# Performance work log

Measured on AMD Instinct MI355X. Metric: run time of the kernel, lower is better.

Reference implementation:

```python
import jax, jax.numpy as jnp
import numpy as np

# LIF constants (LIFParams defaults, normalized units)
V_REST = 0.0
V_TH = 1.0
R = 1.0
DT = 1.0
TAU = 10.0
SLOPE = 5.0  # surrogate heaviside slope

N_INPUT, N_HIDDEN, N_OUTPUT = 784, 256, 10
BATCH, T = 128, 500


def setup_inputs() -> dict:
    key = jax.random.key(0)
    k1, k2, k3 = jax.random.split(key, 3)
    input_spikes = jax.random.uniform(k1, (BATCH, N_INPUT, T), dtype=jnp.float32)
    w_input_hidden = jax.random.uniform(k2, (N_INPUT, N_HIDDEN), dtype=jnp.float32) * 0.1
    w_hidden_output = jax.random.uniform(k3, (N_HIDDEN, N_OUTPUT), dtype=jnp.float32) * 0.1
    return {"input_spikes": input_spikes,
            "w_input_hidden": w_input_hidden,
            "w_hidden_output": w_hidden_output}


def reference(input_spikes, w_input_hidden, w_hidden_output):
    # input_spikes: (B, n_input, T)
    batch = input_spikes.shape[0]
    # relu(weight) computed once (original recomputes per step)
    w_ih = jax.nn.relu(w_input_hidden)
    w_ho = jax.nn.relu(w_hidden_output)
    alpha_h = DT / TAU
    alpha_o = DT / TAU

    xs = jnp.transpose(input_spikes, (2, 0, 1))  # (T, B, n_input)

    def step(carry, x_t):
        v_h, v_o = carry
        I_h = x_t @ w_ih                              # (B, n_hidden)
        v_h = v_h + (-(v_h - V_REST) + R * I_h) * alpha_h
        s_h = jax.nn.sigmoid(SLOPE * (v_h - V_TH))
        I_o = s_h @ w_ho                              # (B, n_output)
        v_o = v_o + (-(v_o - V_REST) + R * I_o) * alpha_o
        s_o = jax.nn.sigmoid(SLOPE * (v_o - V_TH))
        return (v_h, v_o), s_o

    v_h0 = jnp.full((batch, N_HIDDEN), V_REST, dtype=input_spikes.dtype)
    v_o0 = jnp.full((batch, N_OUTPUT), V_REST, dtype=input_spikes.dtype)
    _, out_seq = jax.lax.scan(step, (v_h0, v_o0), xs)   # (T, B, n_output)
    output_spikes = jnp.transpose(out_seq, (1, 2, 0))    # (B, n_output, T)
    firing_rates = output_spikes.mean(axis=2)            # (B, n_output)
    return output_spikes, firing_rates
```

## Files before the change

### kernel.cpp

```cpp
#include <hip/hip_runtime.h>


typedef __attribute__((ext_vector_type(4))) float  floatx4;
typedef __attribute__((ext_vector_type(8))) short  shortx8;
typedef unsigned short u16;
typedef unsigned int   u32;

#define B_   128
#define NIN  784
#define NH   256
#define NO   10
#define T_   500
#define NK   25
#define SROW 520

__device__ __forceinline__ u16 f2bf(float f) {
    union { float f; u32 u; } x; x.f = f;
    u32 r = x.u + 0x7FFFu + ((x.u >> 16) & 1u);
    return (u16)(r >> 16);
}
__device__ __forceinline__ float bf2f(u16 u) {
    union { u32 u; float f; } x; x.u = ((u32)u) << 16; return x.f;
}
__device__ __forceinline__ float sigmoid5(float v) {
    return 1.0f / (1.0f + __expf(-5.0f * (v - 1.0f)));
}

__device__ __forceinline__ void gload16(const u16* g, u16* l) {
    __builtin_amdgcn_global_load_lds(
        (const __attribute__((address_space(1))) unsigned int*)(const void*)g,
        (__attribute__((address_space(3))) unsigned int*)(void*)l, 16, 0, 0);
}

__global__ void convert_W(const float* __restrict__ w_ih,
                          const float* __restrict__ w_ho,
                          u16* __restrict__ Bt, float* __restrict__ wrelu) {
    if (blockIdx.x == NK * 32) {
        for (int i = threadIdx.x; i < NH * NO; i += 256)
            wrelu[i] = fmaxf(0.f, w_ho[i]);
        return;
    }
    const int k = blockIdx.x;
    const int n = threadIdx.x;
    const float f = (k < NIN) ? fmaxf(0.f, w_ih[k * NH + n]) : 0.f;
    const int kt = k >> 5, kk = k & 31;
    const int slot = (kk >> 3) ^ (n & 3) ^ ((n >> 2) & 3);
    Bt[(size_t)kt * 8192 + n * 32 + slot * 8 + (kk & 7)] = f2bf(f);
}

__global__ __launch_bounds__(1024, 4) void gemm_hidden(
    const float* __restrict__ spikes,
    const u16* __restrict__ Bt,
    u16* __restrict__ Ih)
{
    __shared__ u16 SH[32768];
    u16* AS0 = SH;
    u16* AS1 = SH + 8192;
    u16* BS0 = SH + 16384;
    u16* BS1 = SH + 24576;

    const int tid = threadIdx.x;
    const int xcd  = blockIdx.x & 7;
    const int slot = blockIdx.x >> 3;
    const int b    = xcd * 16 + (slot >> 1);
    const int th   = slot & 1;
    const int t0   = th * 256;

    const int kq = tid >> 6, tg = tid & 63;
    const int tloc = t0 + tg * 4;
    const bool t_ok = (tloc <= 496);
    const float* sbase = spikes + (size_t)b * (NIN * T_) + tloc;
    const int oct  = kq >> 2;
    const int koff = (2 * kq) & 7;

    const int lane = tid & 63, wid = tid >> 6;
    const int wm = wid >> 2, wn = wid & 3;
    const int lg = lane >> 4, lr = lane & 15;
    int aOff[4], bOff[4];
#pragma unroll
    for (int mi = 0; mi < 4; ++mi) {
        const int m = wm * 64 + mi * 16 + lr;
        aOff[mi] = m * 32 + ((lg ^ (m & 3) ^ ((m >> 2) & 3)) << 3);
    }
#pragma unroll
    for (int ni = 0; ni < 4; ++ni) {
        const int n = wn * 64 + ni * 16 + lr;
        bOff[ni] = n * 32 + ((lg ^ (n & 3) ^ ((n >> 2) & 3)) << 3);
    }

    floatx4 acc[4][4];
#pragma unroll
    for (int i = 0; i < 4; ++i)
#pragma unroll
        for (int j = 0; j < 4; ++j) acc[i][j] = (floatx4)0.f;

#define LOADA(v0, v1, itv) {                                                   \
        const int gk = (itv) * 32 + 2 * kq;                                    \
        const bool ok0 = t_ok && (gk < NIN);                                   \
        const bool ok1 = t_ok && (gk + 1 < NIN);                               \
        const float* p0 = ok0 ? (sbase + (size_t)gk * T_) : sbase;             \
        const float* p1 = ok1 ? (sbase + (size_t)(gk + 1) * T_) : sbase;       \
        floatx4 u0 = *(const floatx4*)p0;                                      \
        floatx4 u1 = *(const floatx4*)p1;                                      \
        v0 = ok0 ? u0 : (floatx4)0.f;                                          \
        v1 = ok1 ? u1 : (floatx4)0.f; }

#define WRITEA(ASX, v0, v1) { _Pragma("unroll") for (int j = 0; j < 4; ++j) {  \
        const int m = tg * 4 + j;                                              \
        const int slt = oct ^ (m & 3) ^ ((m >> 2) & 3);                        \
        const u32 pk = (u32)f2bf(v0[j]) | ((u32)f2bf(v1[j]) << 16);            \
        *(u32*)&(ASX)[m * 32 + slt * 8 + koff] = pk; } }

#define STAGEB(BSX, itv)                                                       \
        gload16(Bt + (size_t)(itv) * 8192 + tid * 8, (BSX) + tid * 8);

#define MFMAIT(ASX, BSX) { shortx8 af[4], bf[4];                               \
        _Pragma("unroll") for (int mi = 0; mi < 4; ++mi)                       \
            af[mi] = *(const shortx8*)&(ASX)[aOff[mi]];                        \
        _Pragma("unroll") for (int ni = 0; ni < 4; ++ni)                       \
            bf[ni] = *(const shortx8*)&(BSX)[bOff[ni]];                        \
        _Pragma("unroll") for (int mi = 0; mi < 4; ++mi)                       \
        _Pragma("unroll") for (int ni = 0; ni < 4; ++ni)                       \
            acc[mi][ni] = __builtin_amdgcn_mfma_f32_16x16x32_bf16(             \
                af[mi], bf[ni], acc[mi][ni], 0, 0, 0); }

#define CBAR2 { asm volatile("s_waitcnt vmcnt(2) lgkmcnt(0)" ::: "memory");    \
                __builtin_amdgcn_s_barrier(); }
#define LBAR  { asm volatile("s_waitcnt lgkmcnt(0)" ::: "memory");             \
                __builtin_amdgcn_s_barrier(); }

    floatx4 vaP0, vaP1;

    LOADA(vaP0, vaP1, 0);
    WRITEA(AS0, vaP0, vaP1);
    STAGEB(BS0, 0);
    LOADA(vaP0, vaP1, 1);
    CBAR2;

    for (int it = 0; it < 24; it += 2) {
        STAGEB(BS1, it + 1);
        WRITEA(AS1, vaP0, vaP1);
        { const int nv = (it + 2 < 24) ? (it + 2) : 24;
          LOADA(vaP0, vaP1, nv); }
        MFMAIT(AS0, BS0);
        CBAR2;

        STAGEB(BS0, it + 2);
        WRITEA(AS0, vaP0, vaP1);
        { const int nv = (it + 3 < 24) ? (it + 3) : 24;
          LOADA(vaP0, vaP1, nv); }
        MFMAIT(AS1, BS1);
        CBAR2;
    }
    MFMAIT(AS0, BS0);
    LBAR;

    u16* Cs = SH;
#pragma unroll
    for (int h = 0; h < 4; ++h) {
        if (wm == h) {
#pragma unroll
            for (int mi = 0; mi < 4; ++mi)
#pragma unroll
                for (int rr = 0; rr < 2; ++rr) {
                    const int mloc = mi * 16 + lg * 4 + rr * 2;
#pragma unroll
                    for (int ni = 0; ni < 4; ++ni) {
                        const int n = wn * 64 + ni * 16 + lr;
                        const u32 pk = (u32)f2bf(acc[mi][ni][rr * 2]) |
                                       ((u32)f2bf(acc[mi][ni][rr * 2 + 1]) << 16);
                        *(u32*)&Cs[n * 64 + (mloc ^ ((n & 7) << 3))] = pk;
                    }
                }
        }
        LBAR;
        {
            const int n = tid >> 2, ms = tid & 3;
            u16* gdst = Ih + ((size_t)b * 256 + n) * 512 + t0 + h * 64 + ms * 16;
#pragma unroll
            for (int j = 0; j < 2; ++j) {
                const uint4 v = *(const uint4*)&Cs[n * 64 +
                                ((ms * 16 + j * 8) ^ ((n & 7) << 3))];
                *(uint4*)(gdst + j * 8) = v;
            }
        }
        LBAR;
    }
#undef LOADA
#undef WRITEA
#undef STAGEB
#undef MFMAIT
#undef CBAR2
#undef LBAR
}

__global__ __launch_bounds__(512, 2) void scan_dot(
    const u16* __restrict__ Ih,
    const float* __restrict__ wr,
    float* __restrict__ IoP)
{
    __shared__ u16 sbuf[64 * SROW];
    const int tid = threadIdx.x;
    const int hg  = blockIdx.x & 3;
    const int b   = blockIdx.x >> 2;
    const int h0  = hg * 64;
    const int lane = tid & 63, w = tid >> 6;

    for (int r = 0; r < 8; ++r) {
        const int hl = w * 8 + r;
        const u16* p = Ih + ((size_t)b * 256 + h0 + hl) * 512 + lane * 8;
        shortx8 xv = *(const shortx8*)p;
        float I[8];
#pragma unroll
        for (int j = 0; j < 8; ++j) I[j] = bf2f((u16)xv[j]);
        float z = 0.f;
#pragma unroll
        for (int j = 0; j < 8; ++j) z += (I[j] - z) * 0.1f;
        float A = 0.43046721f, Bv = z;
#pragma unroll
        for (int d = 1; d < 64; d <<= 1) {
            const float Au = __shfl_up(A, d);
            const float Bu = __shfl_up(Bv, d);
            if (lane >= d) { Bv = fmaf(A, Bu, Bv); A *= Au; }
        }
        float v = __shfl_up(Bv, 1);
        if (lane == 0) v = 0.f;
        shortx8 sv;
#pragma unroll
        for (int j = 0; j < 8; ++j) {
            v += (I[j] - v) * 0.1f;
            sv[j] = (short)f2bf(sigmoid5(v));
        }
        *(shortx8*)&sbuf[hl * SROW + lane * 8] = sv;
    }
    __syncthreads();

    const int lg = lane >> 4, lr = lane & 15;
    shortx8 bw0, bw1;
#pragma unroll
    for (int j = 0; j < 8; ++j) {
        const int hA = h0 + lg * 8 + j;
        const int hB = hA + 32;
        bw0[j] = (short)((lr < NO) ? f2bf(wr[hA * NO + lr]) : 0);
        bw1[j] = (short)((lr < NO) ? f2bf(wr[hB * NO + lr]) : 0);
    }
#pragma unroll
    for (int fi = 0; fi < 4; ++fi) {
        const int tf = w * 4 + fi;
        const int t  = tf * 16 + lr;
        floatx4 acc = (floatx4)0.f;
#pragma unroll
        for (int ks = 0; ks < 2; ++ks) {
            union { shortx8 s; u32 d[4]; } u;
#pragma unroll
            for (int q = 0; q < 4; ++q) {
                const int h1 = ks * 32 + lg * 8 + 2 * q;
                u.d[q] = (u32)sbuf[h1 * SROW + t] |
                         ((u32)sbuf[(h1 + 1) * SROW + t] << 16);
            }
            acc = __builtin_amdgcn_mfma_f32_16x16x32_bf16(
                u.s, (ks == 0) ? bw0 : bw1, acc, 0, 0, 0);
        }
        if (lr < NO) {
#pragma unroll
            for (int rr = 0; rr < 4; ++rr) {
                const int tt = tf * 16 + lg * 4 + rr;
                IoP[(((size_t)b * 512 + tt) * 4 + hg) * NO + lr] = acc[rr];
            }
        }
    }
}

__global__ __launch_bounds__(256) void lif_out(
    const float* __restrict__ IoP,
    float* __restrict__ out)
{
    __shared__ float Io[T_ * NO];
    __shared__ float vend[25][NO], vstart[25][NO], psum[25][NO];
    const int b = blockIdx.x, tid = threadIdx.x;

    for (int i = tid; i < T_ * NO; i += 256) {
        const int t = i / NO, o = i - t * NO;
        const float* q = IoP + ((size_t)b * 512 + t) * 40 + o;
        Io[i] = (q[0] + q[10]) + (q[20] + q[30]);
    }
    __syncthreads();

    const int seg = tid / NO, o = tid - seg * NO;
    if (tid < 250) {
        float v = 0.f;
#pragma unroll
        for (int j = 0; j < 20; ++j)
            v += (Io[(seg * 20 + j) * NO + o] - v) * 0.1f;
        vend[seg][o] = v;
    }
    __syncthreads();
    if (tid < NO) {
        float vs = 0.f;
#pragma unroll
        for (int sg = 0; sg < 25; ++sg) {
            vstart[sg][tid] = vs;
            vs = vend[sg][tid] + 0.12157665459f * vs;
        }
    }
    __syncthreads();
    if (tid < 250) {
        float v = vstart[seg][o], ps = 0.f;
#pragma unroll
        for (int j = 0; j < 20; ++j) {
            const int t = seg * 20 + j;
            v += (Io[t * NO + o] - v) * 0.1f;
            const float sv = sigmoid5(v);
            out[(size_t)b * (NO * T_) + (size_t)o * T_ + t] = sv;
            ps += sv;
        }
        psum[seg][o] = ps;
    }
    __syncthreads();
    if (tid < NO) {
        float tot = 0.f;
#pragma unroll
        for (int sg = 0; sg < 25; ++sg) tot += psum[sg][tid];
        out[(size_t)(B_ * NO) * T_ + b * NO + tid] = tot * (1.0f / T_);
    }
}

extern "C" void kernel_launch(void* const* d_in, const int* in_sizes, int n_in,
                              void* d_out, int out_size, void* d_ws, size_t ws_size,
                              hipStream_t stream) {
    (void)in_sizes; (void)n_in; (void)out_size; (void)ws_size;
    const float* spikes = (const float*)d_in[0];
    const float* w_ih   = (const float*)d_in[1];
    const float* w_ho   = (const float*)d_in[2];
    float* out = (float*)d_out;

    float* wrelu = (float*)d_ws;
    u16*   Bt    = (u16*)((char*)d_ws + 16384);
    u16*   Ih    = (u16*)((char*)d_ws + 524288);
    float* IoP   = (float*)((char*)d_ws + 524288 + 33554432);

    convert_W  <<<NK * 32 + 1, 256, 0, stream>>>(w_ih, w_ho, Bt, wrelu);
    gemm_hidden<<<256, 1024, 0, stream>>>(spikes, Bt, Ih);
    scan_dot   <<<512, 512, 0, stream>>>(Ih, wrelu, IoP);
    lif_out    <<<B_, 256, 0, stream>>>(IoP, out);
}
```

Before: 82.01 us.

## Double GEMM K-tile to 64 with 8-way XOR swizzle and halved barrier count

The hidden-layer GEMM now processes K in 64-wide tiles instead of 32-wide, so it runs 13 pipelined steps instead of 25. The weight pre-conversion layout and the LDS swizzle change to match (8 slots XORed with row & 7), and each thread now loads four spike rows per stage. The goal is fewer block-wide barriers and more global loads in flight per stage, which should help the memory-bound spike streaming. In exchange, LDS use per block doubles to 128 KB and register pressure rises. The epilogue is also reorganised to write 128-wide time chunks in two passes.

```diff
diff --git a/kernel.cpp b/kernel.cpp
--- a/kernel.cpp
+++ b/kernel.cpp
@@ -11,7 +11,7 @@
 #define NH   256
 #define NO   10
 #define T_   500
-#define NK   25
+#define NK   13
 #define SROW 520
 
 __device__ __forceinline__ u16 f2bf(float f) {
@@ -35,7 +35,7 @@
 __global__ void convert_W(const float* __restrict__ w_ih,
                           const float* __restrict__ w_ho,
                           u16* __restrict__ Bt, float* __restrict__ wrelu) {
-    if (blockIdx.x == NK * 32) {
+    if (blockIdx.x == NK * 64) {
         for (int i = threadIdx.x; i < NH * NO; i += 256)
             wrelu[i] = fmaxf(0.f, w_ho[i]);
         return;
@@ -43,9 +43,9 @@
     const int k = blockIdx.x;
     const int n = threadIdx.x;
     const float f = (k < NIN) ? fmaxf(0.f, w_ih[k * NH + n]) : 0.f;
-    const int kt = k >> 5, kk = k & 31;
-    const int slot = (kk >> 3) ^ (n & 3) ^ ((n >> 2) & 3);
-    Bt[(size_t)kt * 8192 + n * 32 + slot * 8 + (kk & 7)] = f2bf(f);
+    const int kt = k >> 6, kk = k & 63;
+    const int slot = (kk >> 3) ^ (n & 7);
+    Bt[(size_t)kt * 16384 + n * 64 + slot * 8 + (kk & 7)] = f2bf(f);
 }
 
 __global__ __launch_bounds__(1024, 4) void gemm_hidden(
@@ -53,11 +53,11 @@
     const u16* __restrict__ Bt,
     u16* __restrict__ Ih)
 {
-    __shared__ u16 SH[32768];
+    __shared__ u16 SH[65536];
     u16* AS0 = SH;
-    u16* AS1 = SH + 8192;
-    u16* BS0 = SH + 16384;
-    u16* BS1 = SH + 24576;
+    u16* AS1 = SH + 16384;
+    u16* BS0 = SH + 32768;
+    u16* BS1 = SH + 49152;
 
     const int tid = threadIdx.x;
     const int xcd  = blockIdx.x & 7;
@@ -70,22 +70,22 @@
     const int tloc = t0 + tg * 4;
     const bool t_ok = (tloc <= 496);
     const float* sbase = spikes + (size_t)b * (NIN * T_) + tloc;
-    const int oct  = kq >> 2;
-    const int koff = (2 * kq) & 7;
+    const int oct  = kq >> 1;
+    const int koff = (4 * kq) & 7;
 
     const int lane = tid & 63, wid = tid >> 6;
     const int wm = wid >> 2, wn = wid & 3;
     const int lg = lane >> 4, lr = lane & 15;
-    int aOff[4], bOff[4];
+    int mBase[4], mx[4], nBase[4], nx[4];
 #pragma unroll
     for (int mi = 0; mi < 4; ++mi) {
         const int m = wm * 64 + mi * 16 + lr;
-        aOff[mi] = m * 32 + ((lg ^ (m & 3) ^ ((m >> 2) & 3)) << 3);
+        mBase[mi] = m * 64;  mx[mi] = m & 7;
     }
 #pragma unroll
     for (int ni = 0; ni < 4; ++ni) {
         const int n = wn * 64 + ni * 16 + lr;
-        bOff[ni] = n * 32 + ((lg ^ (n & 3) ^ ((n >> 2) & 3)) << 3);
+        nBase[ni] = n * 64;  nx[ni] = n & 7;
     }
 
     floatx4 acc[4][4];
@@ -94,93 +94,94 @@
 #pragma unroll
         for (int j = 0; j < 4; ++j) acc[i][j] = (floatx4)0.f;
 
-#define LOADA(v0, v1, itv) {                                                   \
-        const int gk = (itv) * 32 + 2 * kq;                                    \
-        const bool ok0 = t_ok && (gk < NIN);                                   \
-        const bool ok1 = t_ok && (gk + 1 < NIN);                               \
-        const float* p0 = ok0 ? (sbase + (size_t)gk * T_) : sbase;             \
-        const float* p1 = ok1 ? (sbase + (size_t)(gk + 1) * T_) : sbase;       \
-        floatx4 u0 = *(const floatx4*)p0;                                      \
-        floatx4 u1 = *(const floatx4*)p1;                                      \
-        v0 = ok0 ? u0 : (floatx4)0.f;                                          \
-        v1 = ok1 ? u1 : (floatx4)0.f; }
-
-#define WRITEA(ASX, v0, v1) { _Pragma("unroll") for (int j = 0; j < 4; ++j) {  \
+#define LOADA(va, itv) { _Pragma("unroll") for (int r = 0; r < 4; ++r) {       \
+        const int gk = (itv) * 64 + 4 * kq + r;                                \
+        const bool ok = t_ok && (gk < NIN);                                    \
+        const float* p = ok ? (sbase + (size_t)gk * T_) : sbase;               \
+        floatx4 u = *(const floatx4*)p;                                        \
+        va[r] = ok ? u : (floatx4)0.f; } }
+
+#define WRITEA(ASX, va) { _Pragma("unroll") for (int j = 0; j < 4; ++j) {      \
         const int m = tg * 4 + j;                                              \
-        const int slt = oct ^ (m & 3) ^ ((m >> 2) & 3);                        \
-        const u32 pk = (u32)f2bf(v0[j]) | ((u32)f2bf(v1[j]) << 16);            \
-        *(u32*)&(ASX)[m * 32 + slt * 8 + koff] = pk; } }
-
-#define STAGEB(BSX, itv)                                                       \
-        gload16(Bt + (size_t)(itv) * 8192 + tid * 8, (BSX) + tid * 8);
-
-#define MFMAIT(ASX, BSX) { shortx8 af[4], bf[4];                               \
+        const int slt = oct ^ (m & 7);                                         \
+        uint2 pk;                                                              \
+        pk.x = (u32)f2bf(va[0][j]) | ((u32)f2bf(va[1][j]) << 16);              \
+        pk.y = (u32)f2bf(va[2][j]) | ((u32)f2bf(va[3][j]) << 16);              \
+        *(uint2*)&(ASX)[m * 64 + slt * 8 + koff] = pk; } }
+
+#define STAGEB(BSX, itv) {                                                     \
+        const u16* src = Bt + (size_t)(itv) * 16384;                           \
+        gload16(src + tid * 8,        (BSX) + tid * 8);                        \
+        gload16(src + 8192 + tid * 8, (BSX) + 8192 + tid * 8); }
+
+#define MFMAIT(ASX, BSX) { _Pragma("unroll") for (int ks = 0; ks < 2; ++ks) {  \
+        shortx8 af[4], bf[4];                                                  \
         _Pragma("unroll") for (int mi = 0; mi < 4; ++mi)                       \
-            af[mi] = *(const shortx8*)&(ASX)[aOff[mi]];                        \
+            af[mi] = *(const shortx8*)&(ASX)[mBase[mi] +                       \
+                        (((ks * 4 + lg) ^ mx[mi]) << 3)];                      \
         _Pragma("unroll") for (int ni = 0; ni < 4; ++ni)                       \
-            bf[ni] = *(const shortx8*)&(BSX)[bOff[ni]];                        \
+            bf[ni] = *(const shortx8*)&(BSX)[nBase[ni] +                       \
+                        (((ks * 4 + lg) ^ nx[ni]) << 3)];                      \
         _Pragma("unroll") for (int mi = 0; mi < 4; ++mi)                       \
         _Pragma("unroll") for (int ni = 0; ni < 4; ++ni)                       \
             acc[mi][ni] = __builtin_amdgcn_mfma_f32_16x16x32_bf16(             \
-                af[mi], bf[ni], acc[mi][ni], 0, 0, 0); }
-
-#define CBAR2 { asm volatile("s_waitcnt vmcnt(2) lgkmcnt(0)" ::: "memory");    \
+                af[mi], bf[ni], acc[mi][ni], 0, 0, 0); } }
+
+#define CBAR4 { asm volatile("s_waitcnt vmcnt(4) lgkmcnt(0)" ::: "memory");    \
                 __builtin_amdgcn_s_barrier(); }
 #define LBAR  { asm volatile("s_waitcnt lgkmcnt(0)" ::: "memory");             \
                 __builtin_amdgcn_s_barrier(); }
 
-    floatx4 vaP0, vaP1;
-
-    LOADA(vaP0, vaP1, 0);
-    WRITEA(AS0, vaP0, vaP1);
+    floatx4 vaP[4];
+
+    LOADA(vaP, 0);
+    WRITEA(AS0, vaP);
     STAGEB(BS0, 0);
-    LOADA(vaP0, vaP1, 1);
-    CBAR2;
-
-    for (int it = 0; it < 24; it += 2) {
+    LOADA(vaP, 1);
+    CBAR4;
+
+    for (int it = 0; it < 12; it += 2) {
         STAGEB(BS1, it + 1);
-        WRITEA(AS1, vaP0, vaP1);
-        { const int nv = (it + 2 < 24) ? (it + 2) : 24;
-          LOADA(vaP0, vaP1, nv); }
+        WRITEA(AS1, vaP);
+        LOADA(vaP, it + 2);
         MFMAIT(AS0, BS0);
-        CBAR2;
+        CBAR4;
 
         STAGEB(BS0, it + 2);
-        WRITEA(AS0, vaP0, vaP1);
-        { const int nv = (it + 3 < 24) ? (it + 3) : 24;
-          LOADA(vaP0, vaP1, nv); }
+        WRITEA(AS0, vaP);
+        LOADA(vaP, it + 3);
         MFMAIT(AS1, BS1);
-        CBAR2;
+        CBAR4;
     }
     MFMAIT(AS0, BS0);
     LBAR;
 
     u16* Cs = SH;
 #pragma unroll
-    for (int h = 0; h < 4; ++h) {
-        if (wm == h) {
+    for (int h = 0; h < 2; ++h) {
+        if ((wm >> 1) == h) {
 #pragma unroll
             for (int mi = 0; mi < 4; ++mi)
 #pragma unroll
                 for (int rr = 0; rr < 2; ++rr) {
-                    const int mloc = mi * 16 + lg * 4 + rr * 2;
+                    const int mloc = (wm & 1) * 64 + mi * 16 + lg * 4 + rr * 2;
 #pragma unroll
                     for (int ni = 0; ni < 4; ++ni) {
                         const int n = wn * 64 + ni * 16 + lr;
                         const u32 pk = (u32)f2bf(acc[mi][ni][rr * 2]) |
                                        ((u32)f2bf(acc[mi][ni][rr * 2 + 1]) << 16);
-                        *(u32*)&Cs[n * 64 + (mloc ^ ((n & 7) << 3))] = pk;
+                        *(u32*)&Cs[n * 128 + (mloc ^ ((n & 7) << 3))] = pk;
                     }
                 }
         }
         LBAR;
         {
             const int n = tid >> 2, ms = tid & 3;
-            u16* gdst = Ih + ((size_t)b * 256 + n) * 512 + t0 + h * 64 + ms * 16;
-#pragma unroll
-            for (int j = 0; j < 2; ++j) {
-                const uint4 v = *(const uint4*)&Cs[n * 64 +
-                                ((ms * 16 + j * 8) ^ ((n & 7) << 3))];
+            u16* gdst = Ih + ((size_t)b * 256 + n) * 512 + t0 + h * 128 + ms * 32;
+#pragma unroll
+            for (int j = 0; j < 4; ++j) {
+                const uint4 v = *(const uint4*)&Cs[n * 128 +
+                                ((ms * 32 + j * 8) ^ ((n & 7) << 3))];
                 *(uint4*)(gdst + j * 8) = v;
             }
         }
@@ -190,7 +191,7 @@
 #undef WRITEA
 #undef STAGEB
 #undef MFMAIT
-#undef CBAR2
+#undef CBAR4
 #undef LBAR
 }
 
@@ -339,7 +340,7 @@
     u16*   Ih    = (u16*)((char*)d_ws + 524288);
     float* IoP   = (float*)((char*)d_ws + 524288 + 33554432);
 
-    convert_W  <<<NK * 32 + 1, 256, 0, stream>>>(w_ih, w_ho, Bt, wrelu);
+    convert_W  <<<NK * 64 + 1, 256, 0, stream>>>(w_ih, w_ho, Bt, wrelu);
     gemm_hidden<<<256, 1024, 0, stream>>>(spikes, Bt, Ih);
     scan_dot   <<<512, 512, 0, stream>>>(Ih, wrelu, IoP);
     lif_out    <<<B_, 256, 0, stream>>>(IoP, out);
```

New measurement: 175.6 us. 2.14x slower.
